# Kernel optimization log

Measured on AMD Instinct MI355X. Metric: run time of the kernel, lower is better.

Reference implementation:

```python
import jax, jax.numpy as jnp
import numpy as np

B, N, C = 4, 2048, 768
H = 12
DH = C // H
HID = int(C * 4.0)
SCALE = DH ** -0.5
EPS = 1e-5


def layernorm(x, g, b):
    mu = jnp.mean(x, axis=-1, keepdims=True)
    var = jnp.var(x, axis=-1, keepdims=True)
    return (x - mu) * jax.lax.rsqrt(var + EPS) * g + b


def setup_inputs() -> dict:
    key = jax.random.key(0)
    ks = jax.random.split(key, 10)
    s = lambda fan_in: 1.0 / np.sqrt(fan_in)
    return {
        "x": jax.random.normal(ks[0], (B, N, C), dtype=jnp.float32),
        "ln1_g": jnp.ones((C,), jnp.float32),
        "ln1_b": jnp.zeros((C,), jnp.float32),
        "w_qkv": jax.random.uniform(ks[1], (C, 3 * C), jnp.float32, -s(C), s(C)),
        "w_proj": jax.random.uniform(ks[2], (C, C), jnp.float32, -s(C), s(C)),
        "b_proj": jnp.zeros((C,), jnp.float32),
        "ln2_g": jnp.ones((C,), jnp.float32),
        "ln2_b": jnp.zeros((C,), jnp.float32),
        "w_fc1": jax.random.uniform(ks[3], (C, HID), jnp.float32, -s(C), s(C)),
        "b_fc1": jnp.zeros((HID,), jnp.float32),
        "w_fc2": jax.random.uniform(ks[4], (HID, C), jnp.float32, -s(HID), s(HID)),
        "b_fc2": jnp.zeros((C,), jnp.float32),
    }


def reference(x, ln1_g, ln1_b, w_qkv, w_proj, b_proj, ln2_g, ln2_b, w_fc1, b_fc1, w_fc2, b_fc2):
    # --- attention branch ---
    h = layernorm(x, ln1_g, ln1_b)                       # [B,N,C]
    qkv = (h @ w_qkv).reshape(B, N, 3, H, DH)
    q = qkv[:, :, 0].transpose(0, 2, 1, 3)               # [B,H,N,DH]
    k = qkv[:, :, 1].transpose(0, 2, 1, 3)
    v = qkv[:, :, 2].transpose(0, 2, 1, 3)
    attn = jnp.einsum('bhnd,bhmd->bhnm', q, k) * SCALE   # [B,H,N,N]
    attn = jax.nn.softmax(attn, axis=-1)
    y = jnp.einsum('bhnm,bhmd->bhnd', attn, v)           # [B,H,N,DH]
    y = y.transpose(0, 2, 1, 3).reshape(B, N, C)
    y = y @ w_proj + b_proj
    x = x + y
    # --- MLP branch ---
    h = layernorm(x, ln2_g, ln2_b)
    h = jax.nn.gelu(h @ w_fc1 + b_fc1, approximate=False)
    h = h @ w_fc2 + b_fc2
    return x + h
```

## Files before the change

kernel.cpp:

```cpp
#include <hip/hip_runtime.h>
#include <stdint.h>

#define DEV __device__ __forceinline__

typedef __attribute__((ext_vector_type(8))) short bf16x8;
typedef __attribute__((ext_vector_type(4))) float f32x4;
typedef __attribute__((ext_vector_type(4))) short s16x4;

DEV short f2bf(float f) {
    union { float f; unsigned u; } v; v.f = f;
    unsigned r = v.u + 0x7fffu + ((v.u >> 16) & 1u);
    return (short)(r >> 16);
}

DEV uint32_t cvtpk(float lo, float hi) {
    uint32_t r;
    asm("v_cvt_pk_bf16_f32 %0, %1, %2" : "=v"(r) : "v"(lo), "v"(hi));
    return r;
}

typedef const unsigned int __attribute__((address_space(1)))* gp1;
typedef unsigned int __attribute__((address_space(3)))* lp3;

DEV void gload16(const void* g, void* l) {
    __builtin_amdgcn_global_load_lds((gp1)g, (lp3)l, 16, 0, 0);
}

DEV void wait4_barrier() { asm volatile("s_waitcnt vmcnt(4)\ns_barrier" ::: "memory"); }
DEV void wait2_barrier() { asm volatile("s_waitcnt vmcnt(2)\ns_barrier" ::: "memory"); }
DEV void wait1_barrier() { asm volatile("s_waitcnt vmcnt(1)\ns_barrier" ::: "memory"); }
DEV void wait0_barrier() { asm volatile("s_waitcnt vmcnt(0)\ns_barrier" ::: "memory"); }

__global__ __launch_bounds__(256) void tcvt4(
    const float* __restrict__ W0, short* __restrict__ T0,
    const float* __restrict__ W1, short* __restrict__ T1,
    const float* __restrict__ W2, short* __restrict__ T2,
    const float* __restrict__ W3, short* __restrict__ T3)
{
    __shared__ float t[32][33];
    int bid = blockIdx.x;
    const float* W; short* WT; int K, N, nx, lb;
    if (bid < 1728)      { W = W0; WT = T0; K = 768;  N = 2304; nx = 72; lb = bid; }
    else if (bid < 2304) { W = W1; WT = T1; K = 768;  N = 768;  nx = 24; lb = bid - 1728; }
    else if (bid < 4608) { W = W2; WT = T2; K = 768;  N = 3072; nx = 96; lb = bid - 2304; }
    else                 { W = W3; WT = T3; K = 3072; N = 768;  nx = 24; lb = bid - 4608; }
    int n0 = (lb % nx) * 32, k0 = (lb / nx) * 32;
    int tx = threadIdx.x & 31, ty = threadIdx.x >> 5;
#pragma unroll
    for (int i = 0; i < 32; i += 8)
        t[ty + i][tx] = W[(size_t)(k0 + ty + i) * N + n0 + tx];
    __syncthreads();
#pragma unroll
    for (int i = 0; i < 32; i += 8)
        WT[(size_t)(n0 + ty + i) * K + k0 + tx] = f2bf(t[tx][ty + i]);
}

__global__ __launch_bounds__(256) void ln_bf16(
    const float* __restrict__ x, const float* __restrict__ gam,
    const float* __restrict__ bet, short* __restrict__ out)
{
    const int w = threadIdx.x >> 6, lane = threadIdx.x & 63;
    const size_t row = (size_t)blockIdx.x * 4 + w;
    const float* xr = x + row * 768;
    float4 v[3];
    float s = 0.f, ss = 0.f;
#pragma unroll
    for (int k = 0; k < 3; ++k) {
        v[k] = *(const float4*)(xr + k * 256 + lane * 4);
        s  += v[k].x + v[k].y + v[k].z + v[k].w;
        ss += v[k].x * v[k].x + v[k].y * v[k].y + v[k].z * v[k].z + v[k].w * v[k].w;
    }
#pragma unroll
    for (int i = 1; i < 64; i <<= 1) { s += __shfl_xor(s, i, 64); ss += __shfl_xor(ss, i, 64); }
    const float inv = 1.f / 768.f;
    float mu = s * inv;
    float var = ss * inv - mu * mu;
    float rstd = rsqrtf(var + 1e-5f);
#pragma unroll
    for (int k = 0; k < 3; ++k) {
        int c = k * 256 + lane * 4;
        float vv[4] = { v[k].x, v[k].y, v[k].z, v[k].w };
        s16x4 o;
#pragma unroll
        for (int j = 0; j < 4; ++j)
            o[j] = f2bf((vv[j] - mu) * rstd * gam[c + j] + bet[c + j]);
        *(s16x4*)(out + row * 768 + c) = o;
    }
}

template<int MODE>
DEV void gemm_body(
    const short* __restrict__ A, const short* __restrict__ Bt,
    int M, int N, int K,
    const float* __restrict__ bias, const float* __restrict__ resid,
    float* __restrict__ outf, short* __restrict__ outb,
    short* __restrict__ qo, short* __restrict__ ko, short* __restrict__ vo,
    char* lds)
{
    const int tid = threadIdx.x;
    const int w = tid >> 6, lane = tid & 63;
    const int g = lane >> 4, l15 = lane & 15;
    const int brow = blockIdx.x * 128, bcol = blockIdx.y * 128;
    const int wr = w >> 2, wc = w & 3;
    f32x4 acc[2][2] = {};

    int aoff[2], boff[2];
#pragma unroll
    for (int m = 0; m < 2; ++m) {
        int ra = wr * 32 + m * 16 + l15;
        aoff[m] = ra * 64 + ((g * 16) ^ (((ra >> 1) & 3) << 4));
    }
#pragma unroll
    for (int n = 0; n < 2; ++n) {
        int rb = wc * 32 + n * 16 + l15;
        boff[n] = 8192 + rb * 64 + ((g * 16) ^ (((rb >> 1) & 3) << 4));
    }
    const int dStage = tid * 16;
    const char* pSrc;
    {
        int r = dStage >> 6, b = dStage & 63;
        int bs = b ^ (((r >> 1) & 3) << 4);
        pSrc = (tid < 512)
             ? (const char*)(A  + (size_t)(brow + r) * K) + bs
             : (const char*)(Bt + (size_t)(bcol + (r - 128)) * K) + bs;
    }

#define GSTAGE(BUF, OFF) gload16(pSrc + (OFF), lds + (BUF) * 16384 + dStage)

    const int KT = K >> 5;
    GSTAGE(0, 0);
    GSTAGE(1, 64);
    wait1_barrier();

    const int NM = KT / 3;
    for (int mi = 0; mi < NM; ++mi) {
#pragma unroll
        for (int u = 0; u < 3; ++u) {
            const int s = mi * 3 + u;
            if (s + 2 < KT) GSTAGE((u + 2) % 3, (u + 2) * 64);
            bf16x8 af[2], bfg[2];
#pragma unroll
            for (int m = 0; m < 2; ++m)
                af[m]  = *(const bf16x8*)(lds + u * 16384 + aoff[m]);
#pragma unroll
            for (int n = 0; n < 2; ++n)
                bfg[n] = *(const bf16x8*)(lds + u * 16384 + boff[n]);
#pragma unroll
            for (int m = 0; m < 2; ++m)
#pragma unroll
                for (int n = 0; n < 2; ++n)
                    acc[m][n] = __builtin_amdgcn_mfma_f32_16x16x32_bf16(af[m], bfg[n], acc[m][n], 0, 0, 0);
            if (s + 1 < KT) {
                if (s + 2 < KT) wait1_barrier();
                else            wait0_barrier();
            }
        }
        pSrc += 192;
    }
#undef GSTAGE

#pragma unroll
    for (int m = 0; m < 2; ++m) {
#pragma unroll
        for (int n = 0; n < 2; ++n) {
#pragma unroll
            for (int j = 0; j < 4; ++j) {
                int r = brow + wr * 32 + m * 16 + g * 4 + j;
                int c = bcol + wc * 32 + n * 16 + l15;
                float v = acc[m][n][j];
                if (MODE == 0) {
                    int which = c / 768, cc = c % 768;
                    int h = cc >> 6, d = cc & 63;
                    int b_ = r >> 11, nn = r & 2047;
                    size_t bh = (size_t)b_ * 12 + h;
                    if (which == 0)      qo[(bh * 2048 + nn) * 64 + d] = f2bf(v * 0.18033688011112042f);
                    else if (which == 1) ko[(bh * 2048 + nn) * 64 + d] = f2bf(v);
                    else                 vo[(bh * 64 + d) * 2048 + nn] = f2bf(v);
                } else if (MODE == 1) {
                    outf[(size_t)r * N + c] = v + bias[c] + resid[(size_t)r * N + c];
                } else {
                    float t = v + bias[c];
                    float ge = 0.5f * t * (1.0f + erff(t * 0.70710678118654752f));
                    outb[(size_t)r * N + c] = f2bf(ge);
                }
            }
        }
    }
}

__global__ __launch_bounds__(1024, 8) void g_qkv(
    const short* A, const short* Bt, int M, int N, int K,
    short* qo, short* ko, short* vo)
{
    __shared__ __align__(16) char lds[49152];
    gemm_body<0>(A, Bt, M, N, K, nullptr, nullptr, nullptr, nullptr, qo, ko, vo, lds);
}
__global__ __launch_bounds__(1024, 8) void g_proj(
    const short* A, const short* Bt, int M, int N, int K,
    const float* bias, const float* resid, float* outf)
{
    __shared__ __align__(16) char lds[49152];
    gemm_body<1>(A, Bt, M, N, K, bias, resid, outf, nullptr, nullptr, nullptr, nullptr, lds);
}
__global__ __launch_bounds__(1024, 8) void g_fc1(
    const short* A, const short* Bt, int M, int N, int K,
    const float* bias, short* outb)
{
    __shared__ __align__(16) char lds[49152];
    gemm_body<2>(A, Bt, M, N, K, bias, nullptr, nullptr, outb, nullptr, nullptr, nullptr, lds);
}
__global__ __launch_bounds__(1024, 8) void g_fc2(
    const short* A, const short* Bt, int M, int N, int K,
    const float* bias, const float* resid, float* outf)
{
    __shared__ __align__(16) char lds[49152];
    gemm_body<1>(A, Bt, M, N, K, bias, resid, outf, nullptr, nullptr, nullptr, nullptr, lds);
}

__global__ __launch_bounds__(256, 3) void attn_fwd(
    const short* __restrict__ Q, const short* __restrict__ Kg,
    const short* __restrict__ Vt, short* __restrict__ Y)
{
    __shared__ __align__(16) char alds[43008];
    const int tid = threadIdx.x, w = tid >> 6, lane = tid & 63;
    const int g = lane >> 4, l15 = lane & 15;
    const int bid = blockIdx.y * gridDim.x + blockIdx.x;
    const int nwg = gridDim.x * gridDim.y;
    const int logical = (bid & 7) * (nwg >> 3) + (bid >> 3);
    const int bh = logical >> 4;
    const int q0 = (logical & 15) * 128 + w * 32;
    const short* Qb = Q  + (size_t)bh * 2048 * 64;
    const short* Kb = Kg + (size_t)bh * 2048 * 64;
    const short* Vb = Vt + (size_t)bh * 64 * 2048;

    bf16x8 qf[2][2];
#pragma unroll
    for (int m = 0; m < 2; ++m)
#pragma unroll
        for (int kk = 0; kk < 2; ++kk)
            qf[m][kk] = *(const bf16x8*)(Qb + (size_t)(q0 + m * 16 + l15) * 64 + kk * 32 + g * 8);

    f32x4 accO[2][4] = {};
    float lpart[2] = { 0.f, 0.f };

    int koff[2][2], voff[4], poff[2], pwoff[2][2];
#pragma unroll
    for (int n = 0; n < 2; ++n) {
        int key = n * 16 + l15;
#pragma unroll
        for (int kk = 0; kk < 2; ++kk)
            koff[kk][n] = key * 128 + ((kk * 64 + g * 16) ^ ((key & 7) << 4));
    }
#pragma unroll
    for (int n = 0; n < 4; ++n) {
        int d = n * 16 + l15;
        voff[n] = 16384 + d * 64 + ((g * 16) ^ (((d >> 1) & 3) << 4));
    }
#pragma unroll
    for (int m = 0; m < 2; ++m) {
        int qr = m * 16 + l15;
        poff[m] = 32768 + w * 2560 + qr * 80 + g * 16;
#pragma unroll
        for (int n = 0; n < 2; ++n)
            pwoff[m][n] = 32768 + w * 2560 + qr * 80 + n * 32 + g * 8;
    }
    int dK, dV; const char* pK3; const char* pV3;
    {
        int bb = w * 1024;
        int L = bb + lane * 16;
        int rk = L >> 7, bk_ = L & 127;
        int bsk = bk_ ^ ((rk & 7) << 4);
        dK = bb;
        pK3 = (const char*)(Kb + (size_t)rk * 64) + bsk;
        int rv = L >> 6, bv = L & 63;
        int bsv = bv ^ (((rv >> 1) & 3) << 4);
        dV = bb;
        pV3 = (const char*)(Vb + (size_t)rv * 2048) + bsv;
    }
    gload16(pK3,        alds + dK);
    gload16(pV3,        alds + 16384 + dV);
    gload16(pK3 + 4096, alds + dK + 4096);
    gload16(pV3 + 64,   alds + 16384 + dV + 4096);
    gload16(pK3 + 8192, alds + dK + 8192);
    gload16(pV3 + 128,  alds + 16384 + dV + 8192);
    pK3 += 3 * 4096; pV3 += 3 * 64;
    wait4_barrier();

    for (int tm = 0; tm < 16; ++tm) {
#pragma unroll
        for (int tu = 0; tu < 4; ++tu) {
            const int t = tm * 4 + tu;
            if (t + 3 < 64) {
                gload16(pK3, alds + dK + ((tu + 3) & 3) * 4096);
                gload16(pV3, alds + 16384 + dV + ((tu + 3) & 3) * 4096);
                pK3 += 4096; pV3 += 64;
            }

            f32x4 s2[2][2] = {};
            __builtin_amdgcn_s_setprio(1);
#pragma unroll
            for (int kk = 0; kk < 2; ++kk) {
                bf16x8 kf[2];
#pragma unroll
                for (int n = 0; n < 2; ++n)
                    kf[n] = *(const bf16x8*)(alds + tu * 4096 + koff[kk][n]);
#pragma unroll
                for (int m = 0; m < 2; ++m)
#pragma unroll
                    for (int n = 0; n < 2; ++n)
                        s2[m][n] = __builtin_amdgcn_mfma_f32_16x16x32_bf16(kf[n], qf[m][kk], s2[m][n], 0, 0, 0);
            }
            __builtin_amdgcn_s_setprio(0);

#pragma unroll
            for (int m = 0; m < 2; ++m)
#pragma unroll
                for (int n = 0; n < 2; ++n) {
                    float e0 = __builtin_amdgcn_exp2f(s2[m][n][0]);
                    float e1 = __builtin_amdgcn_exp2f(s2[m][n][1]);
                    float e2 = __builtin_amdgcn_exp2f(s2[m][n][2]);
                    float e3 = __builtin_amdgcn_exp2f(s2[m][n][3]);
                    lpart[m] += (e0 + e1) + (e2 + e3);
                    uint2 pk; pk.x = cvtpk(e0, e1); pk.y = cvtpk(e2, e3);
                    *(uint2*)(alds + pwoff[m][n]) = pk;
                }

            __builtin_amdgcn_s_setprio(1);
            {
                bf16x8 vf[4], pf[2];
#pragma unroll
                for (int n = 0; n < 4; ++n)
                    vf[n] = *(const bf16x8*)(alds + tu * 4096 + voff[n]);
#pragma unroll
                for (int m = 0; m < 2; ++m)
                    pf[m] = *(const bf16x8*)(alds + poff[m]);
#pragma unroll
                for (int m = 0; m < 2; ++m)
#pragma unroll
                    for (int n = 0; n < 4; ++n)
                        accO[m][n] = __builtin_amdgcn_mfma_f32_16x16x32_bf16(pf[m], vf[n], accO[m][n], 0, 0, 0);
            }
            __builtin_amdgcn_s_setprio(0);

            if (t < 61)       wait4_barrier();
            else if (t == 61) wait2_barrier();
            else if (t == 62) wait0_barrier();
        }
    }

#pragma unroll
    for (int m = 0; m < 2; ++m) {
        lpart[m] += __shfl_xor(lpart[m], 16, 64);
        lpart[m] += __shfl_xor(lpart[m], 32, 64);
    }

    int b_ = bh / 12, h = bh % 12;
#pragma unroll
    for (int m = 0; m < 2; ++m) {
        float linv[4];
#pragma unroll
        for (int j = 0; j < 4; ++j)
            linv[j] = 1.0f / __shfl(lpart[m], g * 4 + j, 64);
#pragma unroll
        for (int n = 0; n < 4; ++n)
#pragma unroll
            for (int j = 0; j < 4; ++j) {
                int qq = q0 + m * 16 + g * 4 + j;
                int d = n * 16 + l15;
                Y[((size_t)b_ * 2048 + qq) * 768 + h * 64 + d] = f2bf(accO[m][n][j] * linv[j]);
            }
    }
}

extern "C" void kernel_launch(void* const* d_in, const int* in_sizes, int n_in,
                              void* d_out, int out_size, void* d_ws, size_t ws_size,
                              hipStream_t stream)
{
    const float* x      = (const float*)d_in[0];
    const float* ln1_g  = (const float*)d_in[1];
    const float* ln1_b  = (const float*)d_in[2];
    const float* w_qkv  = (const float*)d_in[3];
    const float* w_proj = (const float*)d_in[4];
    const float* b_proj = (const float*)d_in[5];
    const float* ln2_g  = (const float*)d_in[6];
    const float* ln2_b  = (const float*)d_in[7];
    const float* w_fc1  = (const float*)d_in[8];
    const float* b_fc1  = (const float*)d_in[9];
    const float* w_fc2  = (const float*)d_in[10];
    const float* b_fc2  = (const float*)d_in[11];

    char* ws = (char*)d_ws;
    size_t off = 0;
    auto alloc = [&](size_t bytes) -> void* {
        void* p = ws + off; off += (bytes + 255) & ~(size_t)255; return p;
    };
    short* wqkvT = (short*)alloc((size_t)2304 * 768 * 2);
    short* wprojT= (short*)alloc((size_t)768 * 768 * 2);
    short* wfc1T = (short*)alloc((size_t)3072 * 768 * 2);
    short* wfc2T = (short*)alloc((size_t)768 * 3072 * 2);
    short* h1    = (short*)alloc((size_t)8192 * 768 * 2);
    short* qb    = (short*)alloc((size_t)48 * 2048 * 64 * 2);
    short* kb    = (short*)alloc((size_t)48 * 2048 * 64 * 2);
    short* vtb   = (short*)alloc((size_t)48 * 64 * 2048 * 2);
    short* yb    = (short*)alloc((size_t)8192 * 768 * 2);
    float* X1    = (float*)alloc((size_t)8192 * 768 * 4);
    short* h2    = (short*)alloc((size_t)8192 * 768 * 2);
    short* h3    = (short*)alloc((size_t)8192 * 3072 * 2);

    tcvt4<<<6912, 256, 0, stream>>>(w_qkv, wqkvT, w_proj, wprojT,
                                    w_fc1, wfc1T, w_fc2, wfc2T);

    ln_bf16<<<2048, 256, 0, stream>>>(x, ln1_g, ln1_b, h1);

    g_qkv<<<dim3(64, 18), 1024, 0, stream>>>(h1, wqkvT, 8192, 2304, 768, qb, kb, vtb);

    attn_fwd<<<dim3(16, 48), 256, 0, stream>>>(qb, kb, vtb, yb);

    g_proj<<<dim3(64, 6), 1024, 0, stream>>>(yb, wprojT, 8192, 768, 768, b_proj, x, X1);

    ln_bf16<<<2048, 256, 0, stream>>>(X1, ln2_g, ln2_b, h2);

    g_fc1<<<dim3(64, 24), 1024, 0, stream>>>(h2, wfc1T, 8192, 3072, 768, b_fc1, h3);

    g_fc2<<<dim3(64, 6), 1024, 0, stream>>>(h3, wfc2T, 8192, 768, 3072, b_fc2, X1, (float*)d_out);
}
```

Baseline: 261.9 us.

## Split attention block across 8 waves with 16 query rows each

Reworks the attention kernel so each block runs 8 waves instead of 4, with each wave handling 16 query rows rather than 32. The K/V tile loads are now split by wave role: waves 0-3 load K and waves 4-7 load V, so each thread issues one async LDS load per stage and the vmcnt waits shrink accordingly. The aim is more waves in flight to hide MFMA, exp and LDS latency, and fewer registers per wave. The cost is that each K/V tile in LDS is reused by fewer query rows per wave, and the larger workgroup synchronises more waves at every barrier.

Result: no change. 265.3 us (+1.3%).

```diff
diff --git a/kernel.cpp b/kernel.cpp
--- a/kernel.cpp
+++ b/kernel.cpp
@@ -26,7 +26,6 @@
     __builtin_amdgcn_global_load_lds((gp1)g, (lp3)l, 16, 0, 0);
 }
 
-DEV void wait4_barrier() { asm volatile("s_waitcnt vmcnt(4)\ns_barrier" ::: "memory"); }
 DEV void wait2_barrier() { asm volatile("s_waitcnt vmcnt(2)\ns_barrier" ::: "memory"); }
 DEV void wait1_barrier() { asm volatile("s_waitcnt vmcnt(1)\ns_barrier" ::: "memory"); }
 DEV void wait0_barrier() { asm volatile("s_waitcnt vmcnt(0)\ns_barrier" ::: "memory"); }
@@ -217,7 +216,7 @@
     gemm_body<1>(A, Bt, M, N, K, bias, resid, outf, nullptr, nullptr, nullptr, nullptr, lds);
 }
 
-__global__ __launch_bounds__(256, 3) void attn_fwd(
+__global__ __launch_bounds__(512, 6) void attn_fwd(
     const short* __restrict__ Q, const short* __restrict__ Kg,
     const short* __restrict__ Vt, short* __restrict__ Y)
 {
@@ -228,22 +227,20 @@
     const int nwg = gridDim.x * gridDim.y;
     const int logical = (bid & 7) * (nwg >> 3) + (bid >> 3);
     const int bh = logical >> 4;
-    const int q0 = (logical & 15) * 128 + w * 32;
+    const int q0 = (logical & 15) * 128 + w * 16;
     const short* Qb = Q  + (size_t)bh * 2048 * 64;
     const short* Kb = Kg + (size_t)bh * 2048 * 64;
     const short* Vb = Vt + (size_t)bh * 64 * 2048;
 
-    bf16x8 qf[2][2];
-#pragma unroll
-    for (int m = 0; m < 2; ++m)
-#pragma unroll
-        for (int kk = 0; kk < 2; ++kk)
-            qf[m][kk] = *(const bf16x8*)(Qb + (size_t)(q0 + m * 16 + l15) * 64 + kk * 32 + g * 8);
-
-    f32x4 accO[2][4] = {};
-    float lpart[2] = { 0.f, 0.f };
-
-    int koff[2][2], voff[4], poff[2], pwoff[2][2];
+    bf16x8 qf[2];
+#pragma unroll
+    for (int kk = 0; kk < 2; ++kk)
+        qf[kk] = *(const bf16x8*)(Qb + (size_t)(q0 + l15) * 64 + kk * 32 + g * 8);
+
+    f32x4 accO[4] = {};
+    float lpart = 0.f;
+
+    int koff[2][2], voff[4];
 #pragma unroll
     for (int n = 0; n < 2; ++n) {
         int key = n * 16 + l15;
@@ -256,47 +253,43 @@
         int d = n * 16 + l15;
         voff[n] = 16384 + d * 64 + ((g * 16) ^ (((d >> 1) & 3) << 4));
     }
-#pragma unroll
-    for (int m = 0; m < 2; ++m) {
-        int qr = m * 16 + l15;
-        poff[m] = 32768 + w * 2560 + qr * 80 + g * 16;
-#pragma unroll
-        for (int n = 0; n < 2; ++n)
-            pwoff[m][n] = 32768 + w * 2560 + qr * 80 + n * 32 + g * 8;
-    }
-    int dK, dV; const char* pK3; const char* pV3;
-    {
-        int bb = w * 1024;
-        int L = bb + lane * 16;
+    const int poff = 32768 + w * 1280 + l15 * 80 + g * 16;
+    int pwoff[2];
+#pragma unroll
+    for (int n = 0; n < 2; ++n)
+        pwoff[n] = 32768 + w * 1280 + l15 * 80 + n * 32 + g * 8;
+
+    int dS; const char* pS; int sstep;
+    if (w < 4) {
+        int bb = w * 1024, L = bb + lane * 16;
         int rk = L >> 7, bk_ = L & 127;
-        int bsk = bk_ ^ ((rk & 7) << 4);
-        dK = bb;
-        pK3 = (const char*)(Kb + (size_t)rk * 64) + bsk;
+        dS = bb;
+        pS = (const char*)(Kb + (size_t)rk * 64) + (bk_ ^ ((rk & 7) << 4));
+        sstep = 4096;
+    } else {
+        int bb = (w - 4) * 1024, L = bb + lane * 16;
         int rv = L >> 6, bv = L & 63;
-        int bsv = bv ^ (((rv >> 1) & 3) << 4);
-        dV = bb;
-        pV3 = (const char*)(Vb + (size_t)rv * 2048) + bsv;
-    }
-    gload16(pK3,        alds + dK);
-    gload16(pV3,        alds + 16384 + dV);
-    gload16(pK3 + 4096, alds + dK + 4096);
-    gload16(pV3 + 64,   alds + 16384 + dV + 4096);
-    gload16(pK3 + 8192, alds + dK + 8192);
-    gload16(pV3 + 128,  alds + 16384 + dV + 8192);
-    pK3 += 3 * 4096; pV3 += 3 * 64;
-    wait4_barrier();
+        dS = 16384 + bb;
+        pS = (const char*)(Vb + (size_t)rv * 2048) + (bv ^ (((rv >> 1) & 3) << 4));
+        sstep = 64;
+    }
+
+    gload16(pS,             alds + dS);
+    gload16(pS + sstep,     alds + dS + 4096);
+    gload16(pS + 2 * sstep, alds + dS + 8192);
+    pS += 3 * sstep;
+    wait2_barrier();
 
     for (int tm = 0; tm < 16; ++tm) {
 #pragma unroll
         for (int tu = 0; tu < 4; ++tu) {
             const int t = tm * 4 + tu;
             if (t + 3 < 64) {
-                gload16(pK3, alds + dK + ((tu + 3) & 3) * 4096);
-                gload16(pV3, alds + 16384 + dV + ((tu + 3) & 3) * 4096);
-                pK3 += 4096; pV3 += 64;
-            }
-
-            f32x4 s2[2][2] = {};
+                gload16(pS, alds + dS + ((tu + 3) & 3) * 4096);
+                pS += sstep;
+            }
+
+            f32x4 s2[2] = {};
             __builtin_amdgcn_s_setprio(1);
 #pragma unroll
             for (int kk = 0; kk < 2; ++kk) {
@@ -305,71 +298,55 @@
                 for (int n = 0; n < 2; ++n)
                     kf[n] = *(const bf16x8*)(alds + tu * 4096 + koff[kk][n]);
 #pragma unroll
-                for (int m = 0; m < 2; ++m)
-#pragma unroll
-                    for (int n = 0; n < 2; ++n)
-                        s2[m][n] = __builtin_amdgcn_mfma_f32_16x16x32_bf16(kf[n], qf[m][kk], s2[m][n], 0, 0, 0);
+                for (int n = 0; n < 2; ++n)
+                    s2[n] = __builtin_amdgcn_mfma_f32_16x16x32_bf16(kf[n], qf[kk], s2[n], 0, 0, 0);
             }
             __builtin_amdgcn_s_setprio(0);
 
 #pragma unroll
-            for (int m = 0; m < 2; ++m)
-#pragma unroll
-                for (int n = 0; n < 2; ++n) {
-                    float e0 = __builtin_amdgcn_exp2f(s2[m][n][0]);
-                    float e1 = __builtin_amdgcn_exp2f(s2[m][n][1]);
-                    float e2 = __builtin_amdgcn_exp2f(s2[m][n][2]);
-                    float e3 = __builtin_amdgcn_exp2f(s2[m][n][3]);
-                    lpart[m] += (e0 + e1) + (e2 + e3);
-                    uint2 pk; pk.x = cvtpk(e0, e1); pk.y = cvtpk(e2, e3);
-                    *(uint2*)(alds + pwoff[m][n]) = pk;
-                }
+            for (int n = 0; n < 2; ++n) {
+                float e0 = __builtin_amdgcn_exp2f(s2[n][0]);
+                float e1 = __builtin_amdgcn_exp2f(s2[n][1]);
+                float e2 = __builtin_amdgcn_exp2f(s2[n][2]);
+                float e3 = __builtin_amdgcn_exp2f(s2[n][3]);
+                lpart += (e0 + e1) + (e2 + e3);
+                uint2 pk; pk.x = cvtpk(e0, e1); pk.y = cvtpk(e2, e3);
+                *(uint2*)(alds + pwoff[n]) = pk;
+            }
 
             __builtin_amdgcn_s_setprio(1);
             {
-                bf16x8 vf[4], pf[2];
-#pragma unroll
-                for (int n = 0; n < 4; ++n)
-                    vf[n] = *(const bf16x8*)(alds + tu * 4096 + voff[n]);
-#pragma unroll
-                for (int m = 0; m < 2; ++m)
-                    pf[m] = *(const bf16x8*)(alds + poff[m]);
-#pragma unroll
-                for (int m = 0; m < 2; ++m)
-#pragma unroll
-                    for (int n = 0; n < 4; ++n)
-                        accO[m][n] = __builtin_amdgcn_mfma_f32_16x16x32_bf16(pf[m], vf[n], accO[m][n], 0, 0, 0);
+                bf16x8 pf = *(const bf16x8*)(alds + poff);
+#pragma unroll
+                for (int n = 0; n < 4; ++n) {
+                    bf16x8 vf = *(const bf16x8*)(alds + tu * 4096 + voff[n]);
+                    accO[n] = __builtin_amdgcn_mfma_f32_16x16x32_bf16(pf, vf, accO[n], 0, 0, 0);
+                }
             }
             __builtin_amdgcn_s_setprio(0);
 
-            if (t < 61)       wait4_barrier();
-            else if (t == 61) wait2_barrier();
+            if (t < 61)       wait2_barrier();
+            else if (t == 61) wait1_barrier();
             else if (t == 62) wait0_barrier();
         }
     }
 
-#pragma unroll
-    for (int m = 0; m < 2; ++m) {
-        lpart[m] += __shfl_xor(lpart[m], 16, 64);
-        lpart[m] += __shfl_xor(lpart[m], 32, 64);
-    }
+    lpart += __shfl_xor(lpart, 16, 64);
+    lpart += __shfl_xor(lpart, 32, 64);
 
     int b_ = bh / 12, h = bh % 12;
-#pragma unroll
-    for (int m = 0; m < 2; ++m) {
-        float linv[4];
-#pragma unroll
-        for (int j = 0; j < 4; ++j)
-            linv[j] = 1.0f / __shfl(lpart[m], g * 4 + j, 64);
-#pragma unroll
-        for (int n = 0; n < 4; ++n)
-#pragma unroll
-            for (int j = 0; j < 4; ++j) {
-                int qq = q0 + m * 16 + g * 4 + j;
-                int d = n * 16 + l15;
-                Y[((size_t)b_ * 2048 + qq) * 768 + h * 64 + d] = f2bf(accO[m][n][j] * linv[j]);
-            }
-    }
+    float linv[4];
+#pragma unroll
+    for (int j = 0; j < 4; ++j)
+        linv[j] = 1.0f / __shfl(lpart, g * 4 + j, 64);
+#pragma unroll
+    for (int n = 0; n < 4; ++n)
+#pragma unroll
+        for (int j = 0; j < 4; ++j) {
+            int qq = q0 + g * 4 + j;
+            int d = n * 16 + l15;
+            Y[((size_t)b_ * 2048 + qq) * 768 + h * 64 + d] = f2bf(accO[n][j] * linv[j]);
+        }
 }
 
 extern "C" void kernel_launch(void* const* d_in, const int* in_sizes, int n_in,
@@ -414,7 +391,7 @@
 
     g_qkv<<<dim3(64, 18), 1024, 0, stream>>>(h1, wqkvT, 8192, 2304, 768, qb, kb, vtb);
 
-    attn_fwd<<<dim3(16, 48), 256, 0, stream>>>(qb, kb, vtb, yb);
+    attn_fwd<<<dim3(16, 48), 512, 0, stream>>>(qb, kb, vtb, yb);
 
     g_proj<<<dim3(64, 6), 1024, 0, stream>>>(yb, wprojT, 8192, 768, 768, b_proj, x, X1);
 
```

## Restructure attention K/V pipeline to two tiles per barrier with full drain

Applied to the files above, without the earlier changes.

Replaces the attention kernel's 4-slot K/V ring with a new schedule. The old one prefetched three tiles ahead and placed a partial-vmcnt barrier after every tile. The new one groups tiles in pairs: it loads two slots while computing the other two, then drains all outstanding loads and syncs once per pair. This halves the number of workgroup barriers in the attention main loop. In exchange, prefetch lookahead drops and each barrier waits on every in-flight load, which can expose more global-load latency.

Measured after the change: 262.6 us. Within noise of the previous version (+0.2%).

```diff
diff --git a/kernel.cpp b/kernel.cpp
--- a/kernel.cpp
+++ b/kernel.cpp
@@ -26,8 +26,6 @@
     __builtin_amdgcn_global_load_lds((gp1)g, (lp3)l, 16, 0, 0);
 }
 
-DEV void wait4_barrier() { asm volatile("s_waitcnt vmcnt(4)\ns_barrier" ::: "memory"); }
-DEV void wait2_barrier() { asm volatile("s_waitcnt vmcnt(2)\ns_barrier" ::: "memory"); }
 DEV void wait1_barrier() { asm volatile("s_waitcnt vmcnt(1)\ns_barrier" ::: "memory"); }
 DEV void wait0_barrier() { asm volatile("s_waitcnt vmcnt(0)\ns_barrier" ::: "memory"); }
 
@@ -277,76 +275,70 @@
         dV = bb;
         pV3 = (const char*)(Vb + (size_t)rv * 2048) + bsv;
     }
-    gload16(pK3,        alds + dK);
-    gload16(pV3,        alds + 16384 + dV);
-    gload16(pK3 + 4096, alds + dK + 4096);
-    gload16(pV3 + 64,   alds + 16384 + dV + 4096);
-    gload16(pK3 + 8192, alds + dK + 8192);
-    gload16(pV3 + 128,  alds + 16384 + dV + 8192);
-    pK3 += 3 * 4096; pV3 += 3 * 64;
-    wait4_barrier();
-
-    for (int tm = 0; tm < 16; ++tm) {
-#pragma unroll
-        for (int tu = 0; tu < 4; ++tu) {
-            const int t = tm * 4 + tu;
-            if (t + 3 < 64) {
-                gload16(pK3, alds + dK + ((tu + 3) & 3) * 4096);
-                gload16(pV3, alds + 16384 + dV + ((tu + 3) & 3) * 4096);
-                pK3 += 4096; pV3 += 64;
-            }
-
-            f32x4 s2[2][2] = {};
-            __builtin_amdgcn_s_setprio(1);
-#pragma unroll
-            for (int kk = 0; kk < 2; ++kk) {
-                bf16x8 kf[2];
-#pragma unroll
-                for (int n = 0; n < 2; ++n)
-                    kf[n] = *(const bf16x8*)(alds + tu * 4096 + koff[kk][n]);
-#pragma unroll
-                for (int m = 0; m < 2; ++m)
-#pragma unroll
-                    for (int n = 0; n < 2; ++n)
-                        s2[m][n] = __builtin_amdgcn_mfma_f32_16x16x32_bf16(kf[n], qf[m][kk], s2[m][n], 0, 0, 0);
-            }
-            __builtin_amdgcn_s_setprio(0);
-
-#pragma unroll
-            for (int m = 0; m < 2; ++m)
-#pragma unroll
-                for (int n = 0; n < 2; ++n) {
-                    float e0 = __builtin_amdgcn_exp2f(s2[m][n][0]);
-                    float e1 = __builtin_amdgcn_exp2f(s2[m][n][1]);
-                    float e2 = __builtin_amdgcn_exp2f(s2[m][n][2]);
-                    float e3 = __builtin_amdgcn_exp2f(s2[m][n][3]);
-                    lpart[m] += (e0 + e1) + (e2 + e3);
-                    uint2 pk; pk.x = cvtpk(e0, e1); pk.y = cvtpk(e2, e3);
-                    *(uint2*)(alds + pwoff[m][n]) = pk;
-                }
-
-            __builtin_amdgcn_s_setprio(1);
-            {
-                bf16x8 vf[4], pf[2];
-#pragma unroll
-                for (int n = 0; n < 4; ++n)
-                    vf[n] = *(const bf16x8*)(alds + tu * 4096 + voff[n]);
-#pragma unroll
-                for (int m = 0; m < 2; ++m)
-                    pf[m] = *(const bf16x8*)(alds + poff[m]);
-#pragma unroll
-                for (int m = 0; m < 2; ++m)
-#pragma unroll
-                    for (int n = 0; n < 4; ++n)
-                        accO[m][n] = __builtin_amdgcn_mfma_f32_16x16x32_bf16(pf[m], vf[n], accO[m][n], 0, 0, 0);
-            }
-            __builtin_amdgcn_s_setprio(0);
-
-            if (t < 61)       wait4_barrier();
-            else if (t == 61) wait2_barrier();
-            else if (t == 62) wait0_barrier();
-        }
-    }
+
+#define ASTAGE(SLOT) do { \
+    gload16(pK3, alds + dK + (SLOT) * 4096); \
+    gload16(pV3, alds + 16384 + dV + (SLOT) * 4096); \
+    pK3 += 4096; pV3 += 64; } while (0)
+
+#define ACOMPUTE(SLOT) do { \
+    f32x4 s2[2][2] = {}; \
+    __builtin_amdgcn_s_setprio(1); \
+    _Pragma("unroll") \
+    for (int kk = 0; kk < 2; ++kk) { \
+        bf16x8 kf[2]; \
+        _Pragma("unroll") \
+        for (int n = 0; n < 2; ++n) \
+            kf[n] = *(const bf16x8*)(alds + (SLOT) * 4096 + koff[kk][n]); \
+        _Pragma("unroll") \
+        for (int m = 0; m < 2; ++m) \
+            _Pragma("unroll") \
+            for (int n = 0; n < 2; ++n) \
+                s2[m][n] = __builtin_amdgcn_mfma_f32_16x16x32_bf16(kf[n], qf[m][kk], s2[m][n], 0, 0, 0); \
+    } \
+    __builtin_amdgcn_s_setprio(0); \
+    _Pragma("unroll") \
+    for (int m = 0; m < 2; ++m) \
+        _Pragma("unroll") \
+        for (int n = 0; n < 2; ++n) { \
+            float e0 = __builtin_amdgcn_exp2f(s2[m][n][0]); \
+            float e1 = __builtin_amdgcn_exp2f(s2[m][n][1]); \
+            float e2 = __builtin_amdgcn_exp2f(s2[m][n][2]); \
+            float e3 = __builtin_amdgcn_exp2f(s2[m][n][3]); \
+            lpart[m] += (e0 + e1) + (e2 + e3); \
+            uint2 pk; pk.x = cvtpk(e0, e1); pk.y = cvtpk(e2, e3); \
+            *(uint2*)(alds + pwoff[m][n]) = pk; \
+        } \
+    __builtin_amdgcn_s_setprio(1); \
+    { \
+        bf16x8 vf[4], pf[2]; \
+        _Pragma("unroll") \
+        for (int n = 0; n < 4; ++n) \
+            vf[n] = *(const bf16x8*)(alds + (SLOT) * 4096 + voff[n]); \
+        _Pragma("unroll") \
+        for (int m = 0; m < 2; ++m) \
+            pf[m] = *(const bf16x8*)(alds + poff[m]); \
+        _Pragma("unroll") \
+        for (int m = 0; m < 2; ++m) \
+            _Pragma("unroll") \
+            for (int n = 0; n < 4; ++n) \
+                accO[m][n] = __builtin_amdgcn_mfma_f32_16x16x32_bf16(pf[m], vf[n], accO[m][n], 0, 0, 0); \
+    } \
+    __builtin_amdgcn_s_setprio(0); } while (0)
+
+    ASTAGE(0);
+    ASTAGE(1);
+    wait0_barrier();
+
+    for (int om = 0; om < 15; ++om) {
+        ASTAGE(2); ACOMPUTE(0); ASTAGE(3); ACOMPUTE(1); wait0_barrier();
+        ASTAGE(0); ACOMPUTE(2); ASTAGE(1); ACOMPUTE(3); wait0_barrier();
+    }
+    ASTAGE(2); ACOMPUTE(0); ASTAGE(3); ACOMPUTE(1); wait0_barrier();
+    ACOMPUTE(2); ACOMPUTE(3);
+
+#undef ASTAGE
+#undef ACOMPUTE
 
 #pragma unroll
     for (int m = 0; m < 2; ++m) {
```
